# Performance work log

Hardware: AMD Instinct MI355X
Metric: run time of the kernel (lower is better)

The kernel has to match this reference:

```python
import math
import jax, jax.numpy as jnp
import numpy as np

# ---- static configuration (mirrors init_kwargs / chosen shapes) ----
MUL = 16          # multiplicity in "16x0e+16x1e+16x2e"
B_CFG = 64        # number of configurations in batch
N_ATOM = 64       # atoms per configuration
N_NODES = B_CFG * N_ATOM
N_PAIRS = B_CFG * N_ATOM * N_ATOM

# ---- real Wigner 3j symbols (e3nn convention), computed once in numpy ----
def _su2_cg(j1, m1, j2, m2, j3, m3):
    if m3 != m1 + m2:
        return 0.0
    f = math.factorial
    vmin = max(-j1 + j2 + m3, -j1 + m1, 0)
    vmax = min(j2 + j3 + m1, j3 - j1 + j2, j3 + m3)
    C = math.sqrt((2 * j3 + 1) * f(j3 + j1 - j2) * f(j3 - j1 + j2) * f(j1 + j2 - j3)
                  * f(j3 + m3) * f(j3 - m3)
                  / (f(j1 + j2 + j3 + 1) * f(j1 - m1) * f(j1 + m1) * f(j2 - m2) * f(j2 + m2)))
    S = 0.0
    for v in range(vmin, vmax + 1):
        S += (-1) ** (v + j2 + m2) * f(j2 + j3 + m1 - v) * f(j1 - m1 + v) / (
            f(v) * f(j3 - j1 + j2 - v) * f(j3 + m3 - v) * f(v + j1 - j2 - m3))
    return C * S

def _q_real_to_complex(l):
    q = np.zeros((2 * l + 1, 2 * l + 1), dtype=np.complex128)
    for m in range(-l, 0):
        q[l + m, l + abs(m)] = 1 / 2 ** 0.5
        q[l + m, l - abs(m)] = -1j / 2 ** 0.5
    q[l, l] = 1.0
    for m in range(1, l + 1):
        q[l + m, l + abs(m)] = (-1) ** m / 2 ** 0.5
        q[l + m, l - abs(m)] = 1j * (-1) ** m / 2 ** 0.5
    return (-1j) ** l * q

def _wigner_3j(l1, l2, l3):
    C = np.zeros((2 * l1 + 1, 2 * l2 + 1, 2 * l3 + 1))
    for m1 in range(-l1, l1 + 1):
        for m2 in range(-l2, l2 + 1):
            m3 = m1 + m2
            if abs(m3) <= l3:
                C[l1 + m1, l2 + m2, l3 + m3] = _su2_cg(l1, m1, l2, m2, l3, m3)
    Q1, Q2, Q3 = _q_real_to_complex(l1), _q_real_to_complex(l2), _q_real_to_complex(l3)
    Cr = np.einsum('ij,kl,mn,ikm->jln', Q1, Q2, np.conj(Q3), C.astype(np.complex128))
    assert np.abs(Cr.imag).max() < 1e-6
    Cr = Cr.real
    return Cr / np.linalg.norm(Cr)

# all CG paths (l1, l2, l_out) of the fully connected TP (0e+1e+2e)^2 -> 0e+1e+2e
PATHS = [(0, 0, 0), (1, 1, 0), (2, 2, 0),
         (0, 1, 1), (1, 0, 1), (1, 1, 1), (1, 2, 1), (2, 1, 1), (2, 2, 1),
         (0, 2, 2), (2, 0, 2), (1, 1, 2), (1, 2, 2), (2, 1, 2), (2, 2, 2)]
W3J = {p: _wigner_3j(*p) for p in set(PATHS)}
FAN = {lo: sum(1 for p in PATHS if p[2] == lo) * MUL * MUL for lo in (0, 1, 2)}
ALPHA = {lo: math.sqrt(2 * lo + 1) / math.sqrt(FAN[lo]) for lo in (0, 1, 2)}
# CartesianTensor('ij=ij') change of basis: x_ij = sum_{l,m} QCART[lm,i,j] * irreps[lm]
QCART = np.concatenate([math.sqrt(2 * l + 1) * np.transpose(_wigner_3j(1, 1, l), (2, 0, 1))
                        for l in (0, 1, 2)], axis=0)  # (9, 3, 3), orthonormal rows


def setup_inputs() -> dict:
    key = jax.random.key(0)
    k1, k2 = jax.random.split(key)
    node_feats = jax.random.normal(k1, (N_NODES, MUL * 9), dtype=jnp.float32)
    # layout: for each config, all (i, j) atom pairs with global node indices
    ii, jj = jnp.meshgrid(jnp.arange(N_ATOM, dtype=jnp.int32),
                          jnp.arange(N_ATOM, dtype=jnp.int32), indexing='ij')
    base = (jnp.arange(B_CFG, dtype=jnp.int32) * N_ATOM)[:, None, None]
    rows = (base + ii[None]).reshape(-1)
    cols = (base + jj[None]).reshape(-1)
    layout = jnp.stack([rows, cols], axis=1)  # (N_PAIRS, 2) int32
    tp_weights = jax.random.normal(k2, (len(PATHS), MUL, MUL), dtype=jnp.float32)
    return {'node_feats': node_feats, 'layout': layout, 'tp_weights': tp_weights}


def _split(x):
    # (E, MUL*9) -> {l: (E, MUL, 2l+1)} in irreps order 16x0e | 16x1e | 16x2e
    E = x.shape[0]
    return {0: x[:, :MUL].reshape(E, MUL, 1),
            1: x[:, MUL:4 * MUL].reshape(E, MUL, 3),
            2: x[:, 4 * MUL:].reshape(E, MUL, 5)}


def _forward(node_feats, tp_weights, layout):
    x1 = _split(node_feats[layout[:, 0]])   # gather row atoms
    x2 = _split(node_feats[layout[:, 1]])   # gather column atoms
    E = layout.shape[0]
    dt = node_feats.dtype
    out = {lo: jnp.zeros((E, 2 * lo + 1), dt) for lo in (0, 1, 2)}
    for p, (l1, l2, lo) in enumerate(PATHS):
        w3j = jnp.asarray(W3J[(l1, l2, lo)], dt)
        t = jnp.einsum('eui,uv->evi', x1[l1], tp_weights[p])          # mix multiplicities
        out[lo] = out[lo] + ALPHA[lo] * jnp.einsum('evi,evj,ijk->ek', t, x2[l2], w3j)
    irr = jnp.concatenate([out[0], out[1], out[2]], axis=1)           # (E, 9) = 0e+1e+2e
    cart = jnp.einsum('ek,kij->eij', irr, jnp.asarray(QCART, dt))     # (E, 3, 3)
    # symmetrize: (H + H^T)/2 on the 3n x 3n per-config Hessian
    c = cart.reshape(B_CFG, N_ATOM, N_ATOM, 3, 3)
    c = 0.5 * (c + jnp.transpose(c, (0, 2, 1, 4, 3)))
    return c.reshape(E, 3, 3)


def reference(node_feats, layout, tp_weights):
    return _forward(node_feats, tp_weights, layout)
```

## Files before the change

### kernel.cpp

```cpp
#include <hip/hip_runtime.h>
#include <math.h>


#define NPATH 15

constexpr double cfact(int n){ double r = 1.0; for (int i = 2; i <= n; ++i) r *= (double)i; return r; }
constexpr double csqrt(double x){
  if (x <= 0.0) return 0.0;
  double g = x < 1.0 ? 1.0 : x;
  for (int i = 0; i < 64; ++i) g = 0.5*(g + x/g);
  return g;
}

constexpr double ccg(int j1,int m1,int j2,int m2,int j3,int m3){
  if (m3 != m1 + m2) return 0.0;
  int vmin = -j1 + j2 + m3;
  if (-j1 + m1 > vmin) vmin = -j1 + m1;
  if (0 > vmin) vmin = 0;
  int vmax = j2 + j3 + m1;
  if (j3 - j1 + j2 < vmax) vmax = j3 - j1 + j2;
  if (j3 + m3 < vmax) vmax = j3 + m3;
  double C = csqrt((2.0*j3+1.0)*cfact(j3+j1-j2)*cfact(j3-j1+j2)*cfact(j1+j2-j3)
                   *cfact(j3+m3)*cfact(j3-m3)
                   /(cfact(j1+j2+j3+1)*cfact(j1-m1)*cfact(j1+m1)*cfact(j2-m2)*cfact(j2+m2)));
  double S = 0.0;
  for (int v = vmin; v <= vmax; ++v){
    double term = cfact(j2+j3+m1-v)*cfact(j1-m1+v)
                /(cfact(v)*cfact(j3-j1+j2-v)*cfact(j3+m3-v)*cfact(v+j1-j2-m3));
    S += ((v + j2 + m2) & 1) ? -term : term;
  }
  return C * S;
}

struct QM { double re[5][5]; double im[5][5]; };
constexpr QM cbuild_q(int l){
  QM q{};
  double s = 1.0 / csqrt(2.0);
  for (int m = -l; m < 0; ++m){
    q.re[l+m][l-m] = s;
    q.im[l+m][l+m] = -s;
  }
  q.re[l][l] = 1.0;
  for (int m = 1; m <= l; ++m){
    double sg = (m & 1) ? -1.0 : 1.0;
    q.re[l+m][l+m] = sg * s;
    q.im[l+m][l-m] = sg * s;
  }
  if (l == 1){
    for (int r = 0; r < 5; ++r)
      for (int c = 0; c < 5; ++c){
        double a = q.re[r][c], b = q.im[r][c];
        q.re[r][c] = b; q.im[r][c] = -a;
      }
  } else if (l == 2){
    for (int r = 0; r < 5; ++r)
      for (int c = 0; c < 5; ++c){ q.re[r][c] = -q.re[r][c]; q.im[r][c] = -q.im[r][c]; }
  }
  return q;
}

struct CRP { double v[125]; };
constexpr CRP make_cr(int l1, int l2, int l3){
  QM q1 = cbuild_q(l1), q2 = cbuild_q(l2), q3 = cbuild_q(l3);
  const int d1 = 2*l1+1, d2 = 2*l2+1, d3 = 2*l3+1;
  double CG[125] = {};
  for (int i = 0; i < d1; ++i)
    for (int k = 0; k < d2; ++k)
      for (int m = 0; m < d3; ++m)
        CG[(i*5 + k)*5 + m] = ccg(l1, i-l1, l2, k-l2, l3, m-l3);
  CRP o{};
  for (int j = 0; j < d1; ++j)
    for (int l = 0; l < d2; ++l)
      for (int n = 0; n < d3; ++n){
        double acc = 0.0;
        for (int i = 0; i < d1; ++i)
          for (int k = 0; k < d2; ++k)
            for (int m = 0; m < d3; ++m){
              double c = CG[(i*5 + k)*5 + m];
              if (c == 0.0) continue;
              double are = q1.re[i][j], aim = q1.im[i][j];
              double bre = q2.re[k][l], bim = q2.im[k][l];
              double tre = are*bre - aim*bim;
              double tim = are*bim + aim*bre;
              double cre = q3.re[m][n], cim = q3.im[m][n];
              acc += (tre*cre + tim*cim) * c;
            }
        o.v[(j*d2 + l)*d3 + n] = acc;
      }
  double s2 = 0.0;
  for (int e = 0; e < d1*d2*d3; ++e) s2 += o.v[e]*o.v[e];
  double inv = 1.0 / csqrt(s2);
  for (int e = 0; e < d1*d2*d3; ++e) o.v[e] *= inv;
  return o;
}

constexpr CRP CR0  = make_cr(0,0,0);
constexpr CRP CR1  = make_cr(1,1,0);
constexpr CRP CR2  = make_cr(2,2,0);
constexpr CRP CR3  = make_cr(0,1,1);
constexpr CRP CR4  = make_cr(1,0,1);
constexpr CRP CR5  = make_cr(1,1,1);
constexpr CRP CR6  = make_cr(1,2,1);
constexpr CRP CR7  = make_cr(2,1,1);
constexpr CRP CR8  = make_cr(2,2,1);
constexpr CRP CR9  = make_cr(0,2,2);
constexpr CRP CR10 = make_cr(2,0,2);
constexpr CRP CR11 = make_cr(1,1,2);
constexpr CRP CR12 = make_cr(1,2,2);
constexpr CRP CR13 = make_cr(2,1,2);
constexpr CRP CR14 = make_cr(2,2,2);

struct QCT { double v[81]; };
constexpr QCT make_qc(){
  QCT q{};
  for (int lm = 0; lm < 9; ++lm){
    int l = (lm == 0) ? 0 : ((lm < 4) ? 1 : 2);
    int m = lm - l*l;
    const CRP& cr = (l == 0) ? CR1 : ((l == 1) ? CR5 : CR11);
    double sc = csqrt(2.0*l + 1.0);
    for (int r = 0; r < 9; ++r)
      q.v[lm*9 + r] = cr.v[r*(2*l+1) + m] * sc;
  }
  return q;
}
constexpr QCT QCt = make_qc();

struct WQT { float b8[189*8]; float b1[189]; };
constexpr WQT make_wq(){
  WQT t{};
  const CRP* crs[NPATH] = {&CR0,&CR1,&CR2,&CR3,&CR4,&CR5,&CR6,&CR7,&CR8,&CR9,
                           &CR10,&CR11,&CR12,&CR13,&CR14};
  const int L1[NPATH]   = {0,1,2,0,1,1,1,2,2,0,2,1,1,2,2};
  const int L2[NPATH]   = {0,1,2,1,0,1,2,1,2,2,0,1,2,1,2};
  const int LO[NPATH]   = {0,0,0,1,1,1,1,1,1,2,2,2,2,2,2};
  const int PROW[NPATH] = {0,1,10,35,38,41,50,65,80,105,110,115,124,139,164};
  const double AL[3] = { csqrt(1.0/768.0), csqrt(3.0/1536.0), csqrt(5.0/1536.0) };
  for (int p = 0; p < NPATH; ++p){
    const int d1 = 2*L1[p]+1, d2 = 2*L2[p]+1, d3 = 2*LO[p]+1, lo = LO[p];
    for (int i = 0; i < d1; ++i)
      for (int j = 0; j < d2; ++j)
        for (int a = 0; a < 9; ++a){
          double acc = 0.0;
          for (int m = 0; m < d3; ++m)
            acc += crs[p]->v[(i*d2 + j)*d3 + m] * QCt.v[(lo*lo + m)*9 + a];
          double val = AL[lo] * acc;
          int row = PROW[p] + i*d2 + j;
          if (a < 8) t.b8[row*8 + a] = (float)val;
          else       t.b1[row]       = (float)val;
        }
  }
  return t;
}
__constant__ WQT cWQ = make_wq();

__constant__ int cP_L1[NPATH]   = {0,1,2,0,1,1,1,2,2,0,2,1,1,2,2};
__constant__ int cC2P[51] = {0, 1,1,1, 2,2,2,2,2, 3, 4,4,4, 5,5,5, 6,6,6,
                             7,7,7,7,7, 8,8,8,8,8, 9, 10,10,10,10,10,
                             11,11,11, 12,12,12, 13,13,13,13,13, 14,14,14,14,14};
__constant__ int cC2I[51] = {0, 0,1,2, 0,1,2,3,4, 0, 0,1,2, 0,1,2, 0,1,2,
                             0,1,2,3,4, 0,1,2,3,4, 0, 0,1,2,3,4,
                             0,1,2, 0,1,2, 0,1,2,3,4, 0,1,2,3,4};

#define MQ_STRIDE 1296

#define ACCP(TOFF_, PROW_, D1_)                                              \
  { _Pragma("unroll")                                                        \
    for (int i = 0; i < (D1_); ++i){                                         \
      float tv = pT[((TOFF_) + i) * 16 + v];                                 \
      int row = (PROW_) + i * D2 + j;                                        \
      const float4 m0 = *(const float4*)&sB8[row * 8];                       \
      const float4 m1 = *(const float4*)&sB8[row * 8 + 4];                   \
      const float  m8 = sB1[row];                                            \
      acc[0] += tv*m0.x; acc[1] += tv*m0.y; acc[2] += tv*m0.z;               \
      acc[3] += tv*m0.w; acc[4] += tv*m1.x; acc[5] += tv*m1.y;               \
      acc[6] += tv*m1.z; acc[7] += tv*m1.w; acc[8] += tv*m8;                 \
    } }

__global__ __launch_bounds__(256, 4) void mq_kernel(
    const float* __restrict__ feats,
    const int*   __restrict__ layout,
    const float* __restrict__ tpw,
    float*       __restrict__ mqg)
{
  __shared__ __align__(16) float sB8[189 * 8];
  __shared__ float sB1[192];
  __shared__ __align__(16) float sT[4][816];
  __shared__ __align__(16) float sMq[4][1296];
  const int tid  = threadIdx.x;
  const int wave = tid >> 6;
  const int lane = tid & 63;

  for (int o = tid; o < 1512; o += 256) sB8[o] = cWQ.b8[o];
  if (tid < 189) sB1[tid] = cWQ.b1[tid];

  const int rw = blockIdx.x * 4 + wave;
  int rowNode = layout[2 * (rw * 64)];
  rowNode = __builtin_amdgcn_readfirstlane(rowNode);
  const float* __restrict__ x1 = feats + (size_t)rowNode * 144;

  float* __restrict__ pT = sT[wave];
  {
    const int v  = lane & 15;
    const int cq = lane >> 4;
    for (int it = 0; it < 13; ++it){
      int c = cq + it * 4;
      if (c < 51){
        int p = cC2P[c], i = cC2I[c];
        int l1 = cP_L1[p];
        int st = 2*l1 + 1;
        int loff = (l1 == 0) ? 0 : ((l1 == 1) ? 16 : 64);
        const float* xb = x1 + loff + i;
        const float* wb = tpw + p * 256 + v;
        float s = 0.f;
        #pragma unroll
        for (int u = 0; u < 16; ++u) s += xb[u * st] * wb[u * 16];
        pT[c * 16 + v] = s;
      }
    }
  }

  __syncthreads();

  float* __restrict__ pM = sMq[wave];
  for (int rnd = 0; rnd < 3; ++rnd){
    int c = lane + rnd * 64;
    if (c >= 144) break;
    float acc[9];
    #pragma unroll
    for (int a = 0; a < 9; ++a) acc[a] = 0.f;
    if (c < 16){
      const int v = c, j = 0;
      const int D2 = 1;
      ACCP(0,  0,   1)
      ACCP(10, 38,  3)
      ACCP(30, 110, 5)
    } else if (c < 64){
      const int v = (c - 16) / 3, j = (c - 16) % 3;
      const int D2 = 3;
      ACCP(1,  1,   3)
      ACCP(9,  35,  1)
      ACCP(13, 41,  3)
      ACCP(19, 65,  5)
      ACCP(35, 115, 3)
      ACCP(41, 139, 5)
    } else {
      const int v = (c - 64) / 5, j = (c - 64) % 5;
      const int D2 = 5;
      ACCP(4,  10,  5)
      ACCP(16, 50,  3)
      ACCP(24, 80,  5)
      ACCP(29, 105, 1)
      ACCP(38, 124, 3)
      ACCP(46, 164, 5)
    }
    #pragma unroll
    for (int a = 0; a < 9; ++a) pM[c * 9 + a] = acc[a];
  }

  float* __restrict__ dst = mqg + (size_t)rw * MQ_STRIDE;
  #pragma unroll
  for (int r = 0; r < 6; ++r){
    int idx = lane + r * 64;
    if (idx < 324){
      float4 vv = *(const float4*)(pM + idx * 4);
      *(float4*)(dst + idx * 4) = vv;
    }
  }
}

__global__ __launch_bounds__(256) void cart_kernel(
    const float* __restrict__ feats,
    const int*   __restrict__ layout,
    const float* __restrict__ mqg,
    float*       __restrict__ out)
{
  __shared__ float sX2T[144 * 65];
  __shared__ int   sCol[64];
  __shared__ __align__(16) float sOut[4][576];
  const int tid  = threadIdx.x;
  const int wave = tid >> 6;
  const int lane = tid & 63;
  const int rwBase = blockIdx.x * 4;

  if (tid < 64) sCol[tid] = layout[2 * ((size_t)rwBase * 64 + tid) + 1];
  __syncthreads();

  #pragma unroll
  for (int k = 0; k < 9; ++k){
    int q = k * 256 + tid;
    int j = q / 36, c4 = q - j * 36;
    const float4 xv = *(const float4*)(feats + (size_t)sCol[j] * 144 + c4 * 4);
    int c0 = c4 * 4;
    sX2T[(c0+0)*65 + j] = xv.x;
    sX2T[(c0+1)*65 + j] = xv.y;
    sX2T[(c0+2)*65 + j] = xv.z;
    sX2T[(c0+3)*65 + j] = xv.w;
  }
  __syncthreads();

  const int rw = __builtin_amdgcn_readfirstlane(rwBase + wave);
  const float* __restrict__ mq = mqg + (size_t)rw * MQ_STRIDE;

  float acc[9];
  #pragma unroll
  for (int a = 0; a < 9; ++a) acc[a] = 0.f;

  #pragma unroll 8
  for (int c = 0; c < 144; ++c){
    float x = sX2T[c * 65 + lane];
    #pragma unroll
    for (int a = 0; a < 9; ++a) acc[a] += x * mq[c * 9 + a];
  }

  float* __restrict__ pO = sOut[wave];
  #pragma unroll
  for (int a = 0; a < 9; ++a) pO[lane * 9 + a] = acc[a];
  float* __restrict__ ob = out + (size_t)rw * 576;
  #pragma unroll
  for (int r = 0; r < 3; ++r){
    int idx = lane + r * 64;
    if (idx < 144){
      float4 vv = *(const float4*)(pO + idx * 4);
      *(float4*)(ob + idx * 4) = vv;
    }
  }
}

__global__ __launch_bounds__(256, 4) void fused_kernel(
    const float* __restrict__ feats,
    const int*   __restrict__ layout,
    const float* __restrict__ tpw,
    float*       __restrict__ out)
{
  __shared__ __align__(16) float sB8[189 * 8];
  __shared__ float sB1[192];
  __shared__ __align__(16) float sT[4][816];
  __shared__ __align__(16) float sMqT[4][1296];
  const int tid  = threadIdx.x;
  const int wave = tid >> 6;
  const int lane = tid & 63;

  for (int o = tid; o < 1512; o += 256) sB8[o] = cWQ.b8[o];
  if (tid < 189) sB1[tid] = cWQ.b1[tid];

  const int rw = blockIdx.x * 4 + wave;
  const int e0 = rw * 64;
  int rowNode = layout[2 * e0];
  rowNode = __builtin_amdgcn_readfirstlane(rowNode);
  const float* __restrict__ x1 = feats + (size_t)rowNode * 144;

  float* __restrict__ pT = sT[wave];
  {
    const int v  = lane & 15;
    const int cq = lane >> 4;
    for (int it = 0; it < 13; ++it){
      int c = cq + it * 4;
      if (c < 51){
        int p = cC2P[c], i = cC2I[c];
        int l1 = cP_L1[p];
        int st = 2*l1 + 1;
        int loff = (l1 == 0) ? 0 : ((l1 == 1) ? 16 : 64);
        const float* xb = x1 + loff + i;
        const float* wb = tpw + p * 256 + v;
        float s = 0.f;
        #pragma unroll
        for (int u = 0; u < 16; ++u) s += xb[u * st] * wb[u * 16];
        pT[c * 16 + v] = s;
      }
    }
  }
  __syncthreads();

  float* __restrict__ pM = sMqT[wave];
  for (int rnd = 0; rnd < 3; ++rnd){
    int c = lane + rnd * 64;
    if (c >= 144) break;
    float acc[9];
    #pragma unroll
    for (int a = 0; a < 9; ++a) acc[a] = 0.f;
    if (c < 16){
      const int v = c, j = 0;
      const int D2 = 1;
      ACCP(0,  0,   1)
      ACCP(10, 38,  3)
      ACCP(30, 110, 5)
    } else if (c < 64){
      const int v = (c - 16) / 3, j = (c - 16) % 3;
      const int D2 = 3;
      ACCP(1,  1,   3)
      ACCP(9,  35,  1)
      ACCP(13, 41,  3)
      ACCP(19, 65,  5)
      ACCP(35, 115, 3)
      ACCP(41, 139, 5)
    } else {
      const int v = (c - 64) / 5, j = (c - 64) % 5;
      const int D2 = 5;
      ACCP(4,  10,  5)
      ACCP(16, 50,  3)
      ACCP(24, 80,  5)
      ACCP(29, 105, 1)
      ACCP(38, 124, 3)
      ACCP(46, 164, 5)
    }
    #pragma unroll
    for (int a = 0; a < 9; ++a) pM[a * 144 + c] = acc[a];
  }

  const size_t e = (size_t)e0 + lane;
  const int col = layout[2 * e + 1];
  const float* __restrict__ x2 = feats + (size_t)col * 144;

  float acc[9];
  #pragma unroll
  for (int a = 0; a < 9; ++a) acc[a] = 0.f;

  for (int cc = 0; cc < 36; ++cc){
    const float4 x = *(const float4*)(x2 + cc * 4);
    const float* mb = pM + cc * 4;
    #pragma unroll
    for (int a = 0; a < 9; ++a){
      float4 mv = *(const float4*)(mb + a * 144);
      acc[a] += x.x*mv.x + x.y*mv.y + x.z*mv.z + x.w*mv.w;
    }
  }

  #pragma unroll
  for (int a = 0; a < 9; ++a) pT[lane * 9 + a] = acc[a];
  float* ob = out + (size_t)e0 * 9;
  #pragma unroll
  for (int r = 0; r < 3; ++r){
    int idx = lane + r * 64;
    if (idx < 144){
      float4 vv = *(const float4*)(pT + idx * 4);
      *(float4*)(ob + idx * 4) = vv;
    }
  }
}

__global__ __launch_bounds__(256) void sym_tiled(float* __restrict__ out){
  __shared__ float sA[16 * 145];
  __shared__ float sB[16 * 145];
  const int tid = threadIdx.x;
  const int b  = blockIdx.x / 10;
  const int tp = blockIdx.x - b * 10;
  const int TI[10] = {0,0,0,0,1,1,1,2,2,3};
  const int TJ[10] = {0,1,2,3,1,2,3,2,3,3};
  const int ti = TI[tp], tj = TJ[tp];
  const bool diag = (ti == tj);
  const size_t cfgBase = (size_t)b * 4096 * 9;

  for (int idx = tid; idx < 2304; idx += 256){
    int r = idx / 144, off = idx - r * 144;
    sA[r * 145 + off] = out[cfgBase + ((size_t)(ti*16 + r) * 64 + tj*16) * 9 + off];
  }
  if (!diag){
    for (int idx = tid; idx < 2304; idx += 256){
      int r = idx / 144, off = idx - r * 144;
      sB[r * 145 + off] = out[cfgBase + ((size_t)(tj*16 + r) * 64 + ti*16) * 9 + off];
    }
  }
  __syncthreads();

  const int di = tid >> 4, dj = tid & 15;
  const float* A = sA;
  const float* B = diag ? sA : sB;
  float oa[9], ob[9];
  #pragma unroll
  for (int a = 0; a < 3; ++a)
    #pragma unroll
    for (int d = 0; d < 3; ++d){
      oa[a*3+d] = 0.5f * (A[di*145 + dj*9 + a*3+d] + B[dj*145 + di*9 + d*3+a]);
      if (!diag)
        ob[a*3+d] = 0.5f * (B[di*145 + dj*9 + a*3+d] + A[dj*145 + di*9 + d*3+a]);
    }
  __syncthreads();

  #pragma unroll
  for (int r9 = 0; r9 < 9; ++r9) sA[di*145 + dj*9 + r9] = oa[r9];
  if (!diag){
    #pragma unroll
    for (int r9 = 0; r9 < 9; ++r9) sB[di*145 + dj*9 + r9] = ob[r9];
  }
  __syncthreads();

  for (int idx = tid; idx < 2304; idx += 256){
    int r = idx / 144, off = idx - r * 144;
    out[cfgBase + ((size_t)(ti*16 + r) * 64 + tj*16) * 9 + off] = sA[r * 145 + off];
  }
  if (!diag){
    for (int idx = tid; idx < 2304; idx += 256){
      int r = idx / 144, off = idx - r * 144;
      out[cfgBase + ((size_t)(tj*16 + r) * 64 + ti*16) * 9 + off] = sB[r * 145 + off];
    }
  }
}

extern "C" void kernel_launch(void* const* d_in, const int* in_sizes, int n_in,
                              void* d_out, int out_size, void* d_ws, size_t ws_size,
                              hipStream_t stream) {
  const float* feats  = (const float*)d_in[0];
  const int*   layout = (const int*)  d_in[1];
  const float* tpw    = (const float*)d_in[2];
  float* out = (float*)d_out;
  float* ws  = (float*)d_ws;

  const int E = in_sizes[1] / 2;
  const int R = E / 64;
  const int B = E / 4096;

  const size_t need = (size_t)R * MQ_STRIDE * sizeof(float);
  if (ws_size >= need){
    float* mqg = ws;
    mq_kernel  <<<R / 4, 256, 0, stream>>>(feats, layout, tpw, mqg);
    cart_kernel<<<R / 4, 256, 0, stream>>>(feats, layout, mqg, out);
  } else {
    fused_kernel<<<R / 4, 256, 0, stream>>>(feats, layout, tpw, out);
  }
  sym_tiled<<<B * 10, 256, 0, stream>>>(out);
}
```

Measured before the change: 124.3 us.

## Merge mq and cart kernels into one launch with a shared LDS arena

Combines the two-stage mq/cart pipeline into a single tp_kernel. Each wave writes its Mq matrix to the global workspace, waits on vmcnt, synchronizes the block, then reuses the same LDS buffer (aliased regions) for the transposed column features and reads Mq back from global. This removes one kernel launch and the inter-kernel gap. In exchange it adds a block barrier and a round trip through global memory that is now serialized inside one block, and the larger aliased LDS footprint may reduce occupancy.

```diff
diff --git a/kernel.cpp b/kernel.cpp
--- a/kernel.cpp
+++ b/kernel.cpp
@@ -163,6 +163,15 @@
 
 #define MQ_STRIDE 1296
 
+#define L_B8   0
+#define L_B1   1512
+#define L_T    1704
+#define L_MQ   4968
+#define L_X2   0
+#define L_OUT  9360
+#define L_COL  11664
+#define L_TOT  11728
+
 #define ACCP(TOFF_, PROW_, D1_)                                              \
   { _Pragma("unroll")                                                        \
     for (int i = 0; i < (D1_); ++i){                                         \
@@ -176,29 +185,33 @@
       acc[6] += tv*m1.z; acc[7] += tv*m1.w; acc[8] += tv*m8;                 \
     } }
 
-__global__ __launch_bounds__(256, 4) void mq_kernel(
+__global__ __launch_bounds__(256) void tp_kernel(
     const float* __restrict__ feats,
     const int*   __restrict__ layout,
     const float* __restrict__ tpw,
-    float*       __restrict__ mqg)
+    float*       __restrict__ mqw,
+    const float* __restrict__ mqr,
+    float*       __restrict__ out)
 {
-  __shared__ __align__(16) float sB8[189 * 8];
-  __shared__ float sB1[192];
-  __shared__ __align__(16) float sT[4][816];
-  __shared__ __align__(16) float sMq[4][1296];
+  __shared__ __align__(16) float lds[L_TOT];
+  float* sB8 = lds + L_B8;
+  float* sB1 = lds + L_B1;
+  int*   sCol = (int*)(lds + L_COL);
   const int tid  = threadIdx.x;
   const int wave = tid >> 6;
   const int lane = tid & 63;
+  const int rwBase = blockIdx.x * 4;
+  const int rw = rwBase + wave;
 
   for (int o = tid; o < 1512; o += 256) sB8[o] = cWQ.b8[o];
   if (tid < 189) sB1[tid] = cWQ.b1[tid];
-
-  const int rw = blockIdx.x * 4 + wave;
+  if (tid < 64)  sCol[tid] = layout[2 * ((size_t)rwBase * 64 + tid) + 1];
+
   int rowNode = layout[2 * (rw * 64)];
   rowNode = __builtin_amdgcn_readfirstlane(rowNode);
   const float* __restrict__ x1 = feats + (size_t)rowNode * 144;
 
-  float* __restrict__ pT = sT[wave];
+  float* pT = lds + L_T + wave * 816;
   {
     const int v  = lane & 15;
     const int cq = lane >> 4;
@@ -221,7 +234,7 @@
 
   __syncthreads();
 
-  float* __restrict__ pM = sMq[wave];
+  float* pM = lds + L_MQ + wave * 1296;
   for (int rnd = 0; rnd < 3; ++rnd){
     int c = lane + rnd * 64;
     if (c >= 144) break;
@@ -257,49 +270,39 @@
     for (int a = 0; a < 9; ++a) pM[c * 9 + a] = acc[a];
   }
 
-  float* __restrict__ dst = mqg + (size_t)rw * MQ_STRIDE;
-  #pragma unroll
-  for (int r = 0; r < 6; ++r){
-    int idx = lane + r * 64;
-    if (idx < 324){
-      float4 vv = *(const float4*)(pM + idx * 4);
-      *(float4*)(dst + idx * 4) = vv;
-    }
-  }
-}
-
-__global__ __launch_bounds__(256) void cart_kernel(
-    const float* __restrict__ feats,
-    const int*   __restrict__ layout,
-    const float* __restrict__ mqg,
-    float*       __restrict__ out)
-{
-  __shared__ float sX2T[144 * 65];
-  __shared__ int   sCol[64];
-  __shared__ __align__(16) float sOut[4][576];
-  const int tid  = threadIdx.x;
-  const int wave = tid >> 6;
-  const int lane = tid & 63;
-  const int rwBase = blockIdx.x * 4;
-
-  if (tid < 64) sCol[tid] = layout[2 * ((size_t)rwBase * 64 + tid) + 1];
-  __syncthreads();
-
-  #pragma unroll
-  for (int k = 0; k < 9; ++k){
-    int q = k * 256 + tid;
-    int j = q / 36, c4 = q - j * 36;
-    const float4 xv = *(const float4*)(feats + (size_t)sCol[j] * 144 + c4 * 4);
-    int c0 = c4 * 4;
-    sX2T[(c0+0)*65 + j] = xv.x;
-    sX2T[(c0+1)*65 + j] = xv.y;
-    sX2T[(c0+2)*65 + j] = xv.z;
-    sX2T[(c0+3)*65 + j] = xv.w;
-  }
-  __syncthreads();
-
-  const int rw = __builtin_amdgcn_readfirstlane(rwBase + wave);
-  const float* __restrict__ mq = mqg + (size_t)rw * MQ_STRIDE;
+  {
+    float* dst = mqw + (size_t)rw * MQ_STRIDE;
+    #pragma unroll
+    for (int r = 0; r < 6; ++r){
+      int idx = lane + r * 64;
+      if (idx < 324){
+        float4 vv = *(const float4*)(pM + idx * 4);
+        *(float4*)(dst + idx * 4) = vv;
+      }
+    }
+  }
+  __asm__ __volatile__("s_waitcnt vmcnt(0)" ::: "memory");
+
+  __syncthreads();
+
+  {
+    float* sX2 = lds + L_X2;
+    #pragma unroll
+    for (int k = 0; k < 9; ++k){
+      int q = k * 256 + tid;
+      int j = q / 36, c4 = q - j * 36;
+      const float4 xv = *(const float4*)(feats + (size_t)sCol[j] * 144 + c4 * 4);
+      int c0 = c4 * 4;
+      sX2[(c0+0)*65 + j] = xv.x;
+      sX2[(c0+1)*65 + j] = xv.y;
+      sX2[(c0+2)*65 + j] = xv.z;
+      sX2[(c0+3)*65 + j] = xv.w;
+    }
+  }
+  __syncthreads();
+
+  const float* mq = mqr + (size_t)rw * MQ_STRIDE;
+  const float* sX2 = lds + L_X2;
 
   float acc[9];
   #pragma unroll
@@ -307,21 +310,23 @@
 
   #pragma unroll 8
   for (int c = 0; c < 144; ++c){
-    float x = sX2T[c * 65 + lane];
+    float x = sX2[c * 65 + lane];
     #pragma unroll
     for (int a = 0; a < 9; ++a) acc[a] += x * mq[c * 9 + a];
   }
 
-  float* __restrict__ pO = sOut[wave];
-  #pragma unroll
-  for (int a = 0; a < 9; ++a) pO[lane * 9 + a] = acc[a];
-  float* __restrict__ ob = out + (size_t)rw * 576;
-  #pragma unroll
-  for (int r = 0; r < 3; ++r){
-    int idx = lane + r * 64;
-    if (idx < 144){
-      float4 vv = *(const float4*)(pO + idx * 4);
-      *(float4*)(ob + idx * 4) = vv;
+  {
+    float* pO = lds + L_OUT + wave * 576;
+    #pragma unroll
+    for (int a = 0; a < 9; ++a) pO[lane * 9 + a] = acc[a];
+    float* ob = out + (size_t)rw * 576;
+    #pragma unroll
+    for (int r = 0; r < 3; ++r){
+      int idx = lane + r * 64;
+      if (idx < 144){
+        float4 vv = *(const float4*)(pO + idx * 4);
+        *(float4*)(ob + idx * 4) = vv;
+      }
     }
   }
 }
@@ -511,9 +516,7 @@
 
   const size_t need = (size_t)R * MQ_STRIDE * sizeof(float);
   if (ws_size >= need){
-    float* mqg = ws;
-    mq_kernel  <<<R / 4, 256, 0, stream>>>(feats, layout, tpw, mqg);
-    cart_kernel<<<R / 4, 256, 0, stream>>>(feats, layout, mqg, out);
+    tp_kernel<<<R / 4, 256, 0, stream>>>(feats, layout, tpw, ws, ws, out);
   } else {
     fused_kernel<<<R / 4, 256, 0, stream>>>(feats, layout, tpw, out);
   }
```

New measurement: 138.8 us. +11.6%, slower.
